# Performance work log

Hardware: AMD Instinct MI355X
Metric: run time of the kernel (lower is better)

The kernel has to match this reference:

```python
import jax, jax.numpy as jnp
import numpy as np

B, S, D = 4, 4096, 256


def setup_inputs() -> dict:
    key = jax.random.key(0)
    ks = jax.random.split(key, 7)
    s = 1.0 / np.sqrt(D)
    return {
        "x": jax.random.normal(ks[0], (B, S, D), dtype=jnp.float32),
        "Wq": jax.random.normal(ks[1], (D, D), dtype=jnp.float32) * s,
        "bq": jax.random.normal(ks[2], (D,), dtype=jnp.float32) * s,
        "Wk": jax.random.normal(ks[3], (D, D), dtype=jnp.float32) * s,
        "bk": jax.random.normal(ks[4], (D,), dtype=jnp.float32) * s,
        "Wv": jax.random.normal(ks[5], (D, D), dtype=jnp.float32) * s,
        "bv": jax.random.normal(ks[6], (D,), dtype=jnp.float32) * s,
    }


def reference(x, Wq, bq, Wk, bk, Wv, bv):
    # QKV projections (torch Linear: y = x @ W^T + b; here W stored as [in, out])
    Q = jax.nn.relu(jnp.einsum("bsd,df->bsf", x, Wq) + bq)  # [B,S,D]
    K = jax.nn.relu(jnp.einsum("bsd,df->bsf", x, Wk) + bk)  # [B,S,D]
    V = jnp.einsum("bsd,df->bsf", x, Wv) + bv               # [B,S,D]
    scores = jnp.einsum("bqd,bkd->bqk", Q, K)               # [B,S,S], no 1/sqrt(d) scaling (as in source)
    attn = jax.nn.softmax(scores, axis=-1)
    return jnp.einsum("bqk,bkd->bqd", attn, V)              # [B,S,D]
```

## Files before the change

### kernel.cpp

```cpp
#include <hip/hip_runtime.h>
#include <stdint.h>

typedef __bf16 bf16;
typedef bf16 bf16x8 __attribute__((ext_vector_type(8)));
typedef _Float16 f16;
typedef f16 f16x8 __attribute__((ext_vector_type(8)));
typedef f16 f16x4 __attribute__((ext_vector_type(4)));
typedef float f32x4 __attribute__((ext_vector_type(4)));
typedef float f32x16 __attribute__((ext_vector_type(16)));
typedef unsigned short u16;
typedef unsigned int u32;
typedef u32 u32x2 __attribute__((ext_vector_type(2)));
typedef u16 u16x8v __attribute__((ext_vector_type(8)));

__device__ __forceinline__ u16 f2bf(float f) {
  u32 u = __float_as_uint(f);
  u32 r = u + 0x7fffu + ((u >> 16) & 1u);
  return (u16)(r >> 16);
}
__device__ __forceinline__ float bf2f(u16 h) { return __uint_as_float(((u32)h) << 16); }

__device__ __forceinline__ u32 pkrtz(float a, float b) {
  auto r = __builtin_amdgcn_cvt_pkrtz(a, b);
  u32 u; __builtin_memcpy(&u, &r, 4);
  return u;
}

union ABu { u16x8v u; bf16x8 b; };
union PAu { u32 w[4]; f16x8 v; };

__global__ void wt_kernel(const float* __restrict__ Wq, const float* __restrict__ Wk,
                          const float* __restrict__ Wv, u16* __restrict__ Wh,
                          u16* __restrict__ Wl) {
  int w = blockIdx.x >> 4;
  int chunk = blockIdx.x & 15;
  const float* W = (w == 0) ? Wq : (w == 1) ? Wk : Wv;
  int t = threadIdx.x;
  int o = chunk * 16 + (t & 15);
  int i0 = (t >> 4) * 16;
  u16x8v h0, h1, l0, l1;
  #pragma unroll
  for (int ii = 0; ii < 8; ++ii) {
    float v0 = W[(size_t)(i0 + ii) * 256 + o];
    u16 h = f2bf(v0); h0[ii] = h; l0[ii] = f2bf(v0 - bf2f(h));
    float v1 = W[(size_t)(i0 + 8 + ii) * 256 + o];
    h = f2bf(v1); h1[ii] = h; l1[ii] = f2bf(v1 - bf2f(h));
  }
  size_t base = (size_t)w * 65536 + (size_t)o * 256 + i0;
  *(u16x8v*)(Wh + base) = h0; *(u16x8v*)(Wh + base + 8) = h1;
  *(u16x8v*)(Wl + base) = l0; *(u16x8v*)(Wl + base + 8) = l1;
}

__global__ __launch_bounds__(256, 2) void proj_kernel(
    const float* __restrict__ x, const float* __restrict__ bq,
    const float* __restrict__ bk, const float* __restrict__ bv,
    const u16* __restrict__ Wh, const u16* __restrict__ Wl,
    f16* __restrict__ Qf, f16* __restrict__ Kf, f16* __restrict__ Vt) {
  __shared__ __align__(16) char Whs[16384];
  __shared__ __align__(16) char Wls[16384];

  int m = blockIdx.x, w = blockIdx.y;
  int tid = threadIdx.x, lane = tid & 63, wv = tid >> 6;
  int r = lane & 15, c = lane >> 4;
  int row0 = m * 128 + wv * 32;
  const char* Whw = (const char*)(Wh + (size_t)w * 65536);
  const char* Wlw = (const char*)(Wl + (size_t)w * 65536);
  const float* bias = (w == 0) ? bq : (w == 1) ? bk : bv;

  f32x4 acc[2][16];
  #pragma unroll
  for (int g = 0; g < 2; ++g)
    #pragma unroll
    for (int n = 0; n < 16; ++n) acc[g][n] = (f32x4)0.0f;

  for (int ks = 0; ks < 8; ++ks) {
    if (ks) __syncthreads();
    #pragma unroll
    for (int ss = 0; ss < 4; ++ss) {
      int slot = ss * 256 + tid;
      int row = slot >> 2, c4 = slot & 3;
      int dby = (c4 << 4) ^ (((row >> 1) & 3) << 4);
      const char* gh = Whw + (size_t)row * 512 + ks * 64 + dby;
      const char* gl = Wlw + (size_t)row * 512 + ks * 64 + dby;
      __builtin_amdgcn_global_load_lds(
          (const __attribute__((address_space(1))) void*)gh,
          (__attribute__((address_space(3))) void*)(Whs + slot * 16), 16, 0, 0);
      __builtin_amdgcn_global_load_lds(
          (const __attribute__((address_space(1))) void*)gl,
          (__attribute__((address_space(3))) void*)(Wls + slot * 16), 16, 0, 0);
    }
    __syncthreads();

    ABu ah[2], al[2];
    #pragma unroll
    for (int g = 0; g < 2; ++g) {
      const float* xrow = x + (size_t)(row0 + g * 16 + r) * 256 + ks * 32 + c * 8;
      float4 a0 = *(const float4*)(xrow);
      float4 a1 = *(const float4*)(xrow + 4);
      float xv[8] = {a0.x, a0.y, a0.z, a0.w, a1.x, a1.y, a1.z, a1.w};
      #pragma unroll
      for (int j = 0; j < 8; ++j) {
        u16 h = f2bf(xv[j]);
        ah[g].u[j] = h;
        al[g].u[j] = f2bf(xv[j] - bf2f(h));
      }
    }
    #pragma unroll
    for (int n = 0; n < 16; ++n) {
      int wrow = n * 16 + r;
      int wof = (c * 16) ^ (((wrow >> 1) & 3) << 4);
      bf16x8 whf = *(const bf16x8*)(Whs + wrow * 64 + wof);
      bf16x8 wlf = *(const bf16x8*)(Wls + wrow * 64 + wof);
      #pragma unroll
      for (int g = 0; g < 2; ++g) {
        acc[g][n] = __builtin_amdgcn_mfma_f32_16x16x32_bf16(ah[g].b, whf, acc[g][n], 0, 0, 0);
        acc[g][n] = __builtin_amdgcn_mfma_f32_16x16x32_bf16(al[g].b, whf, acc[g][n], 0, 0, 0);
        acc[g][n] = __builtin_amdgcn_mfma_f32_16x16x32_bf16(ah[g].b, wlf, acc[g][n], 0, 0, 0);
      }
    }
  }

  if (w < 2) {
    f16* outp = (w == 0) ? Qf : Kf;
    #pragma unroll
    for (int g = 0; g < 2; ++g)
      #pragma unroll
      for (int n = 0; n < 16; ++n) {
        int col = n * 16 + r;
        float bb = bias[col];
        #pragma unroll
        for (int i = 0; i < 4; ++i) {
          float v = fmaxf(acc[g][n][i] + bb, 0.0f);
          outp[(size_t)(row0 + g * 16 + c * 4 + i) * 256 + col] = (f16)v;
        }
      }
  } else {
    #pragma unroll
    for (int g = 0; g < 2; ++g) {
      int grow = row0 + g * 16 + c * 4;
      int b = grow >> 12, s0 = grow & 4095;
      #pragma unroll
      for (int n = 0; n < 16; ++n) {
        int d = n * 16 + r;
        float bb = bias[d];
        f16x4 pk;
        #pragma unroll
        for (int i = 0; i < 4; ++i) pk[i] = (f16)(acc[g][n][i] + bb);
        *(f16x4*)(Vt + (size_t)(b * 256 + d) * 4096 + s0) = pk;
      }
    }
  }
}

__global__ __launch_bounds__(512, 2) void attn_kernel(
    const f16* __restrict__ Qf, const f16* __restrict__ Kf,
    const f16* __restrict__ Vt, f16* __restrict__ Opart, float* __restrict__ Ml) {
  __shared__ __align__(16) char Ksm[2][32768];
  __shared__ __align__(16) char Vsm[2][32768];

  int bid = blockIdx.x;
  int xcd = bid & 7;
  int batch = xcd >> 1;
  int kq = ((xcd & 1) << 1) | ((bid >> 3) & 1);
  int qtl = bid >> 4;
  int tid = threadIdx.x, lane = tid & 63, wv = tid >> 6;
  int ln = lane & 31, hi = lane >> 5;
  int q0 = qtl * 256 + wv * 32;
  int kv0 = kq * 1024;

  f16x8 qf[16];
  {
    const f16* qp = Qf + ((size_t)(batch * 4096 + q0 + ln)) * 256 + hi * 8;
    #pragma unroll
    for (int ks = 0; ks < 16; ++ks) qf[ks] = *(const f16x8*)(qp + ks * 16);
  }

  f32x16 O[8];
  #pragma unroll
  for (int dt = 0; dt < 8; ++dt) O[dt] = (f32x16)0.0f;
  float m_ = -1.0e30f, l_ = 0.0f;

  const char* Kbase = (const char*)(Kf + ((size_t)(batch * 4096 + kv0)) * 256);
  const char* Vbase = (const char*)(Vt + (size_t)batch * 1048576 + kv0);

#define STAGE(T, BF)                                                           \
  {                                                                            \
    _Pragma("unroll")                                                          \
    for (int rr = 0; rr < 4; ++rr) {                                           \
      int slot = rr * 512 + tid;                                               \
      int krow = slot >> 5;                                                    \
      int dby = ((slot & 31) << 4) ^ ((krow & 7) << 4);                        \
      const char* g = Kbase + (size_t)((T) * 64 + krow) * 512 + dby;           \
      __builtin_amdgcn_global_load_lds(                                        \
          (const __attribute__((address_space(1))) void*)g,                    \
          (__attribute__((address_space(3))) void*)(Ksm[BF] + slot * 16), 16, 0, 0); \
    }                                                                          \
    _Pragma("unroll")                                                          \
    for (int rr = 0; rr < 4; ++rr) {                                           \
      int slot = rr * 512 + tid;                                               \
      int vrow = slot >> 3;                                                    \
      int dby = ((slot & 7) << 4) ^ ((vrow & 7) << 4);                         \
      const char* g = Vbase + (size_t)vrow * 8192 + (T) * 128 + dby;           \
      __builtin_amdgcn_global_load_lds(                                        \
          (const __attribute__((address_space(1))) void*)g,                    \
          (__attribute__((address_space(3))) void*)(Vsm[BF] + slot * 16), 16, 0, 0); \
    }                                                                          \
  }

  int kswz = (ln & 7) << 4;
  int vswz = (ln & 7) << 4;
  int hi16 = hi * 16;

#define SOFTMAX(SA, PA0, PA1)                                                  \
  {                                                                            \
    float pm = fmaxf(                                                          \
        fmaxf(fmaxf(fmaxf(SA[0], SA[1]), fmaxf(SA[2], SA[3])),                 \
              fmaxf(fmaxf(SA[4], SA[5]), fmaxf(SA[6], SA[7]))),                \
        fmaxf(fmaxf(fmaxf(SA[8], SA[9]), fmaxf(SA[10], SA[11])),               \
              fmaxf(fmaxf(SA[12], SA[13]), fmaxf(SA[14], SA[15]))));           \
    pm = fmaxf(pm, __shfl_xor(pm, 32));                                        \
    if (!__all(pm <= m_ + 8.0f)) {                                             \
      float mn = fmaxf(m_, pm);                                                \
      float sc = __expf(m_ - mn);                                              \
      m_ = mn; l_ *= sc;                                                       \
      _Pragma("unroll")                                                        \
      for (int rg = 0; rg < 16; ++rg) {                                        \
        float srg = __shfl(sc, (rg & 3) + 8 * (rg >> 2) + 4 * hi);             \
        _Pragma("unroll")                                                      \
        for (int dt = 0; dt < 8; ++dt) O[dt][rg] *= srg;                       \
      }                                                                        \
    }                                                                          \
    float p_[16];                                                              \
    _Pragma("unroll")                                                          \
    for (int j = 0; j < 16; ++j) p_[j] = __expf(SA[j] - m_);                   \
    float ps = (((p_[0] + p_[1]) + (p_[2] + p_[3])) +                          \
                ((p_[4] + p_[5]) + (p_[6] + p_[7]))) +                         \
               (((p_[8] + p_[9]) + (p_[10] + p_[11])) +                        \
                ((p_[12] + p_[13]) + (p_[14] + p_[15])));                      \
    ps += __shfl_xor(ps, 32);                                                  \
    l_ += ps;                                                                  \
    {                                                                          \
      u32x2 r1 = __builtin_amdgcn_permlane32_swap(pkrtz(p_[0], p_[1]), pkrtz(p_[4], p_[5]), false, false); \
      u32x2 r2 = __builtin_amdgcn_permlane32_swap(pkrtz(p_[2], p_[3]), pkrtz(p_[6], p_[7]), false, false); \
      PA0.w[0] = r1[0]; PA0.w[1] = r2[0]; PA0.w[2] = r1[1]; PA0.w[3] = r2[1];  \
      u32x2 r3 = __builtin_amdgcn_permlane32_swap(pkrtz(p_[8], p_[9]), pkrtz(p_[12], p_[13]), false, false); \
      u32x2 r4 = __builtin_amdgcn_permlane32_swap(pkrtz(p_[10], p_[11]), pkrtz(p_[14], p_[15]), false, false); \
      PA1.w[0] = r3[0]; PA1.w[1] = r4[0]; PA1.w[2] = r3[1]; PA1.w[3] = r4[1];  \
    }                                                                          \
  }

  STAGE(0, 0);

  for (int t = 0; t < 16; ++t) {
    __builtin_amdgcn_s_barrier();
    if (t < 15) {
      STAGE(t + 1, (t + 1) & 1);
      asm volatile("s_waitcnt vmcnt(8)" ::: "memory");
    } else {
      asm volatile("s_waitcnt vmcnt(0)" ::: "memory");
    }
    __builtin_amdgcn_sched_barrier(0);
    __builtin_amdgcn_s_barrier();

    const char* Kc = Ksm[t & 1];
    const char* Vc = Vsm[t & 1];

    f32x16 sA = (f32x16)0.0f;
    __builtin_amdgcn_s_setprio(1);
    #pragma unroll
    for (int ks = 0; ks < 16; ++ks) {
      f16x8 kf = *(const f16x8*)(Kc + ln * 512 + ((ks * 32 + hi16) ^ kswz));
      sA = __builtin_amdgcn_mfma_f32_32x32x16_f16(kf, qf[ks], sA, 0, 0, 0);
    }
    __builtin_amdgcn_s_setprio(0);
    PAu paA0, paA1;
    SOFTMAX(sA, paA0, paA1);

    f32x16 sB = (f32x16)0.0f;
    __builtin_amdgcn_s_setprio(1);
    #pragma unroll
    for (int ks = 0; ks < 16; ++ks) {
      f16x8 kf = *(const f16x8*)(Kc + (32 + ln) * 512 + ((ks * 32 + hi16) ^ kswz));
      sB = __builtin_amdgcn_mfma_f32_32x32x16_f16(kf, qf[ks], sB, 0, 0, 0);
      int dt = ks >> 1, k2 = ks & 1;
      f16x8 vf = *(const f16x8*)(Vc + (dt * 32 + ln) * 128 + ((k2 * 32 + hi16) ^ vswz));
      O[dt] = __builtin_amdgcn_mfma_f32_32x32x16_f16(k2 ? paA1.v : paA0.v, vf, O[dt], 0, 0, 0);
    }
    __builtin_amdgcn_s_setprio(0);
    PAu paB0, paB1;
    SOFTMAX(sB, paB0, paB1);

    __builtin_amdgcn_s_setprio(1);
    #pragma unroll
    for (int ks = 0; ks < 16; ++ks) {
      int dt = ks >> 1, k2 = ks & 1;
      f16x8 vf = *(const f16x8*)(Vc + (dt * 32 + ln) * 128 + ((64 + k2 * 32 + hi16) ^ vswz));
      O[dt] = __builtin_amdgcn_mfma_f32_32x32x16_f16(k2 ? paB1.v : paB0.v, vf, O[dt], 0, 0, 0);
    }
    __builtin_amdgcn_s_setprio(0);
  }

  float invl = 1.0f / l_;
  #pragma unroll
  for (int rg = 0; rg < 16; ++rg) {
    int qr = (rg & 3) + 8 * (rg >> 2) + 4 * hi;
    float iv = __shfl(invl, qr);
    size_t row = (size_t)kq * 16384 + batch * 4096 + q0 + qr;
    #pragma unroll
    for (int dt = 0; dt < 8; ++dt)
      Opart[row * 256 + dt * 32 + ln] = (f16)(O[dt][rg] * iv);
  }
  if (hi == 0) {
    size_t grow = (size_t)kq * 16384 + batch * 4096 + q0 + ln;
    Ml[grow * 2] = m_;
    Ml[grow * 2 + 1] = l_;
  }
#undef STAGE
#undef SOFTMAX
}

__global__ __launch_bounds__(256) void merge_kernel(
    const f16* __restrict__ Opart, const float* __restrict__ Ml,
    float* __restrict__ out) {
  int gid = blockIdx.x * 256 + threadIdx.x;
  int row = gid >> 5, d0 = (gid & 31) * 8;
  float m[4], l[4];
  #pragma unroll
  for (int p = 0; p < 4; ++p) {
    m[p] = Ml[((size_t)p * 16384 + row) * 2];
    l[p] = Ml[((size_t)p * 16384 + row) * 2 + 1];
  }
  float M = fmaxf(fmaxf(m[0], m[1]), fmaxf(m[2], m[3]));
  float wl[4], L = 0.f;
  #pragma unroll
  for (int p = 0; p < 4; ++p) { wl[p] = __expf(m[p] - M) * l[p]; L += wl[p]; }
  float o[8] = {0.f, 0.f, 0.f, 0.f, 0.f, 0.f, 0.f, 0.f};
  #pragma unroll
  for (int p = 0; p < 4; ++p) {
    f16x8 v = *(const f16x8*)(Opart + ((size_t)p * 16384 + row) * 256 + d0);
    #pragma unroll
    for (int j = 0; j < 8; ++j) o[j] += wl[p] * (float)v[j];
  }
  float invL = 1.0f / L;
  float4 o0 = {o[0] * invL, o[1] * invL, o[2] * invL, o[3] * invL};
  float4 o1 = {o[4] * invL, o[5] * invL, o[6] * invL, o[7] * invL};
  *(float4*)(out + (size_t)row * 256 + d0) = o0;
  *(float4*)(out + (size_t)row * 256 + d0 + 4) = o1;
}

extern "C" void kernel_launch(void* const* d_in, const int* in_sizes, int n_in,
                              void* d_out, int out_size, void* d_ws, size_t ws_size,
                              hipStream_t stream) {
  const float* x  = (const float*)d_in[0];
  const float* Wq = (const float*)d_in[1];
  const float* bq = (const float*)d_in[2];
  const float* Wk = (const float*)d_in[3];
  const float* bk = (const float*)d_in[4];
  const float* Wv = (const float*)d_in[5];
  const float* bv = (const float*)d_in[6];
  float* out = (float*)d_out;

  u16* Wh = (u16*)d_ws;
  u16* Wl = Wh + 3 * 65536;
  f16* Qf = (f16*)(Wl + 3 * 65536);
  f16* Kf = Qf + (size_t)16384 * 256;
  f16* Vt = Kf + (size_t)16384 * 256;
  f16* Opart = Vt + (size_t)4 * 256 * 4096;
  float* Ml = (float*)(Opart + (size_t)4 * 16384 * 256);

  wt_kernel<<<48, 256, 0, stream>>>(Wq, Wk, Wv, Wh, Wl);
  proj_kernel<<<dim3(128, 3), 256, 0, stream>>>(x, bq, bk, bv, Wh, Wl, Qf, Kf, Vt);
  attn_kernel<<<256, 512, 0, stream>>>(Qf, Kf, Vt, Opart, Ml);
  merge_kernel<<<2048, 256, 0, stream>>>(Opart, Ml, out);
}
```

Baseline: 157.4 us.

## Fold log2e into Q, use exp2 softmax, permlane reductions, stagger K halves per wave

```diff
diff --git a/kernel.cpp b/kernel.cpp
--- a/kernel.cpp
+++ b/kernel.cpp
@@ -13,6 +13,8 @@
 typedef u32 u32x2 __attribute__((ext_vector_type(2)));
 typedef u16 u16x8v __attribute__((ext_vector_type(8)));
 
+#define LOG2E 1.44269504088896340736f
+
 __device__ __forceinline__ u16 f2bf(float f) {
   u32 u = __float_as_uint(f);
   u32 r = u + 0x7fffu + ((u >> 16) & 1u);
@@ -24,6 +26,14 @@
   auto r = __builtin_amdgcn_cvt_pkrtz(a, b);
   u32 u; __builtin_memcpy(&u, &r, 4);
   return u;
+}
+__device__ __forceinline__ float xmax32(float v) {
+  u32x2 r = __builtin_amdgcn_permlane32_swap(__float_as_uint(v), __float_as_uint(v), false, false);
+  return fmaxf(__uint_as_float(r[0]), __uint_as_float(r[1]));
+}
+__device__ __forceinline__ float xsum32(float v) {
+  u32x2 r = __builtin_amdgcn_permlane32_swap(__float_as_uint(v), __float_as_uint(v), false, false);
+  return __uint_as_float(r[0]) + __uint_as_float(r[1]);
 }
 
 union ABu { u16x8v u; bf16x8 b; };
@@ -122,6 +132,7 @@
 
   if (w < 2) {
     f16* outp = (w == 0) ? Qf : Kf;
+    float osc = (w == 0) ? LOG2E : 1.0f;
     #pragma unroll
     for (int g = 0; g < 2; ++g)
       #pragma unroll
@@ -130,7 +141,7 @@
         float bb = bias[col];
         #pragma unroll
         for (int i = 0; i < 4; ++i) {
-          float v = fmaxf(acc[g][n][i] + bb, 0.0f);
+          float v = fmaxf(acc[g][n][i] + bb, 0.0f) * osc;
           outp[(size_t)(row0 + g * 16 + c * 4 + i) * 256 + col] = (f16)v;
         }
       }
@@ -167,6 +178,7 @@
   int ln = lane & 31, hi = lane >> 5;
   int q0 = qtl * 256 + wv * 32;
   int kv0 = kq * 1024;
+  int par = wv & 1;
 
   f16x8 qf[16];
   {
@@ -210,6 +222,8 @@
   int kswz = (ln & 7) << 4;
   int vswz = (ln & 7) << 4;
   int hi16 = hi * 16;
+  int kbA = par * 32;
+  int kbB = 32 - kbA;
 
 #define SOFTMAX(SA, PA0, PA1)                                                  \
   {                                                                            \
@@ -218,10 +232,10 @@
               fmaxf(fmaxf(SA[4], SA[5]), fmaxf(SA[6], SA[7]))),                \
         fmaxf(fmaxf(fmaxf(SA[8], SA[9]), fmaxf(SA[10], SA[11])),               \
               fmaxf(fmaxf(SA[12], SA[13]), fmaxf(SA[14], SA[15]))));           \
-    pm = fmaxf(pm, __shfl_xor(pm, 32));                                        \
-    if (!__all(pm <= m_ + 8.0f)) {                                             \
+    pm = xmax32(pm);                                                           \
+    if (!__all(pm <= m_ + 11.5416f)) {       \
       float mn = fmaxf(m_, pm);                                                \
-      float sc = __expf(m_ - mn);                                              \
+      float sc = exp2f(m_ - mn);                                               \
       m_ = mn; l_ *= sc;                                                       \
       _Pragma("unroll")                                                        \
       for (int rg = 0; rg < 16; ++rg) {                                        \
@@ -232,13 +246,12 @@
     }                                                                          \
     float p_[16];                                                              \
     _Pragma("unroll")                                                          \
-    for (int j = 0; j < 16; ++j) p_[j] = __expf(SA[j] - m_);                   \
+    for (int j = 0; j < 16; ++j) p_[j] = exp2f(SA[j] - m_);                    \
     float ps = (((p_[0] + p_[1]) + (p_[2] + p_[3])) +                          \
                 ((p_[4] + p_[5]) + (p_[6] + p_[7]))) +                         \
                (((p_[8] + p_[9]) + (p_[10] + p_[11])) +                        \
                 ((p_[12] + p_[13]) + (p_[14] + p_[15])));                      \
-    ps += __shfl_xor(ps, 32);                                                  \
-    l_ += ps;                                                                  \
+    l_ += xsum32(ps);                                                          \
     {                                                                          \
       u32x2 r1 = __builtin_amdgcn_permlane32_swap(pkrtz(p_[0], p_[1]), pkrtz(p_[4], p_[5]), false, false); \
       u32x2 r2 = __builtin_amdgcn_permlane32_swap(pkrtz(p_[2], p_[3]), pkrtz(p_[6], p_[7]), false, false); \
@@ -264,12 +277,15 @@
 
     const char* Kc = Ksm[t & 1];
     const char* Vc = Vsm[t & 1];
+    const char* KcA = Kc + kbA * 512;
+    const char* KcB = Kc + kbB * 512;
+    int vbA = kbA * 2, vbB = kbB * 2;
 
     f32x16 sA = (f32x16)0.0f;
     __builtin_amdgcn_s_setprio(1);
     #pragma unroll
     for (int ks = 0; ks < 16; ++ks) {
-      f16x8 kf = *(const f16x8*)(Kc + ln * 512 + ((ks * 32 + hi16) ^ kswz));
+      f16x8 kf = *(const f16x8*)(KcA + ln * 512 + ((ks * 32 + hi16) ^ kswz));
       sA = __builtin_amdgcn_mfma_f32_32x32x16_f16(kf, qf[ks], sA, 0, 0, 0);
     }
     __builtin_amdgcn_s_setprio(0);
@@ -280,10 +296,10 @@
     __builtin_amdgcn_s_setprio(1);
     #pragma unroll
     for (int ks = 0; ks < 16; ++ks) {
-      f16x8 kf = *(const f16x8*)(Kc + (32 + ln) * 512 + ((ks * 32 + hi16) ^ kswz));
+      f16x8 kf = *(const f16x8*)(KcB + ln * 512 + ((ks * 32 + hi16) ^ kswz));
       sB = __builtin_amdgcn_mfma_f32_32x32x16_f16(kf, qf[ks], sB, 0, 0, 0);
       int dt = ks >> 1, k2 = ks & 1;
-      f16x8 vf = *(const f16x8*)(Vc + (dt * 32 + ln) * 128 + ((k2 * 32 + hi16) ^ vswz));
+      f16x8 vf = *(const f16x8*)(Vc + (dt * 32 + ln) * 128 + ((vbA + k2 * 32 + hi16) ^ vswz));
       O[dt] = __builtin_amdgcn_mfma_f32_32x32x16_f16(k2 ? paA1.v : paA0.v, vf, O[dt], 0, 0, 0);
     }
     __builtin_amdgcn_s_setprio(0);
@@ -294,7 +310,7 @@
     #pragma unroll
     for (int ks = 0; ks < 16; ++ks) {
       int dt = ks >> 1, k2 = ks & 1;
-      f16x8 vf = *(const f16x8*)(Vc + (dt * 32 + ln) * 128 + ((64 + k2 * 32 + hi16) ^ vswz));
+      f16x8 vf = *(const f16x8*)(Vc + (dt * 32 + ln) * 128 + ((vbB + k2 * 32 + hi16) ^ vswz));
       O[dt] = __builtin_amdgcn_mfma_f32_32x32x16_f16(k2 ? paB1.v : paB0.v, vf, O[dt], 0, 0, 0);
     }
     __builtin_amdgcn_s_setprio(0);
@@ -333,7 +349,7 @@
   float M = fmaxf(fmaxf(m[0], m[1]), fmaxf(m[2], m[3]));
   float wl[4], L = 0.f;
   #pragma unroll
-  for (int p = 0; p < 4; ++p) { wl[p] = __expf(m[p] - M) * l[p]; L += wl[p]; }
+  for (int p = 0; p < 4; ++p) { wl[p] = exp2f(m[p] - M) * l[p]; L += wl[p]; }
   float o[8] = {0.f, 0.f, 0.f, 0.f, 0.f, 0.f, 0.f, 0.f};
   #pragma unroll
   for (int p = 0; p < 4; ++p) {
```

Result: faster. 153.8 us, median of 2 (-2.3%).
